# Kernel tuning notes

Hardware: AMD Instinct MI355X
Metric: run time of the kernel (lower is better)

## Reference

```python
import jax, jax.numpy as jnp
import numpy as np

N_KERNELS = 5
MUL_FACTOR = 2.0


def setup_inputs() -> dict:
    key = jax.random.key(0)
    X = jax.random.normal(key, (4096, 64), dtype=jnp.float32)
    # bandwidth multipliers: mul_factor ** (arange(K) - K//2)
    bandwidth_multipliers = (MUL_FACTOR ** (jnp.arange(N_KERNELS) - N_KERNELS // 2)).astype(jnp.float32)
    return {"X": X, "bandwidth_multipliers": bandwidth_multipliers}


def reference(X, bandwidth_multipliers):
    # squared pairwise euclidean distances: ||x_i||^2 + ||x_j||^2 - 2 x_i . x_j
    sq_norms = jnp.sum(X * X, axis=-1)                      # [N]
    gram = X @ X.T                                          # [N, N]
    L2 = jnp.maximum(sq_norms[:, None] + sq_norms[None, :] - 2.0 * gram, 0.0)  # [N, N]

    # bandwidth estimate uses .data in torch -> stop_gradient
    n = X.shape[0]
    bw = jax.lax.stop_gradient(L2.sum()) / (n * n - n)

    # sum over K bandwidth-scaled RBF kernels
    scales = bw * bandwidth_multipliers                     # [K]
    out = jnp.sum(jnp.exp(-L2[None, :, :] / scales[:, None, None]), axis=0)  # [N, N]
    return out
```

## Files before the change

kernel.cpp:

```cpp
#include <hip/hip_runtime.h>
#include <hip/hip_bf16.h>
#include <math.h>

#define N 4096
#define PB 32

typedef __attribute__((ext_vector_type(8))) short short8;
typedef __attribute__((ext_vector_type(4))) float floatx4;

__device__ float g_ws[PB * 66];
__device__ float g_nrm[N];
__device__ uint4 g_X[N * 8];

__device__ inline unsigned bfpk(float a, float b) {
    unsigned ua = __float_as_uint(a), ub = __float_as_uint(b);
    ua = (ua + 0x7fffu + ((ua >> 16) & 1u)) >> 16;
    ub = (ub + 0x7fffu + ((ub >> 16) & 1u)) >> 16;
    return ua | (ub << 16);
}

__device__ inline uint4 pack8(float4 f0, float4 f1) {
    uint4 r;
    r.x = bfpk(f0.x, f0.y);
    r.y = bfpk(f0.z, f0.w);
    r.z = bfpk(f1.x, f1.y);
    r.w = bfpk(f1.z, f1.w);
    return r;
}

__global__ __launch_bounds__(256) void prep_kernel(const float* __restrict__ X) {
    __shared__ float sm[256];
    __shared__ float ssum[4];
    const int lane = threadIdx.x & 63, w = threadIdx.x >> 6;
    const int b = blockIdx.x;

    const int row0 = b * 128 + w * 32;
    float mloc = 0.f, Sloc = 0.f;
    #pragma unroll
    for (int rr = 0; rr < 32; ++rr) {
        float x = X[(size_t)(row0 + rr) * 64 + lane];
        mloc += x; Sloc += x * x;
    }
    sm[threadIdx.x] = mloc;
    #pragma unroll
    for (int off = 1; off < 64; off <<= 1) Sloc += __shfl_xor(Sloc, off, 64);
    if (lane == 0) ssum[w] = Sloc;
    __syncthreads();
    if (threadIdx.x < 64) {
        g_ws[b * 66 + threadIdx.x] =
            sm[threadIdx.x] + sm[64 + threadIdx.x] + sm[128 + threadIdx.x] + sm[192 + threadIdx.x];
    } else if (threadIdx.x == 64) {
        g_ws[b * 66 + 64] = ssum[0] + ssum[1] + ssum[2] + ssum[3];
    }

    const int r = b * 128 + (threadIdx.x >> 1);
    const int h = threadIdx.x & 1;
    const float4* pr = (const float4*)(X + (size_t)r * 64 + h * 32);
    float4 f0 = pr[0], f1 = pr[1], f2 = pr[2], f3 = pr[3];
    float4 f4 = pr[4], f5 = pr[5], f6 = pr[6], f7 = pr[7];
    float nh = f0.x*f0.x + f0.y*f0.y + f0.z*f0.z + f0.w*f0.w
             + f1.x*f1.x + f1.y*f1.y + f1.z*f1.z + f1.w*f1.w
             + f2.x*f2.x + f2.y*f2.y + f2.z*f2.z + f2.w*f2.w
             + f3.x*f3.x + f3.y*f3.y + f3.z*f3.z + f3.w*f3.w
             + f4.x*f4.x + f4.y*f4.y + f4.z*f4.z + f4.w*f4.w
             + f5.x*f5.x + f5.y*f5.y + f5.z*f5.z + f5.w*f5.w
             + f6.x*f6.x + f6.y*f6.y + f6.z*f6.z + f6.w*f6.w
             + f7.x*f7.x + f7.y*f7.y + f7.z*f7.z + f7.w*f7.w;
    nh += __shfl_xor(nh, 1, 64);
    if (h == 0) g_nrm[r] = nh;
    const int sw = r & 7;
    g_X[r * 8 + ((4*h + 0) ^ sw)] = pack8(f0, f1);
    g_X[r * 8 + ((4*h + 1) ^ sw)] = pack8(f2, f3);
    g_X[r * 8 + ((4*h + 2) ^ sw)] = pack8(f4, f5);
    g_X[r * 8 + ((4*h + 3) ^ sw)] = pack8(f6, f7);
}

__global__ __launch_bounds__(256) void rbf_kernel(float* __restrict__ out) {
    __shared__ uint4 lB[1024];

    const int t_ = threadIdx.x;
    const int b  = blockIdx.x;

    int I, J, h;
    if (b < 64) {
        I = J = b >> 1; h = b & 1;
    } else {
        int t = (b - 64) >> 1; h = (b - 64) & 1;
        int i = (int)((63.0f - sqrtf((float)(3969 - 8 * t))) * 0.5f);
        while (31 * (i + 1) - ((i + 1) * i) / 2 <= t) ++i;
        while (31 * i - (i * (i - 1)) / 2 > t) --i;
        int oi = 31 * i - (i * (i - 1)) / 2;
        I = i; J = i + 1 + (t - oi);
    }
    const int rowBase = I * 128 + h * 64;
    const int colBase = J * 128;
    const bool offdiag = (I != J);

    #pragma unroll
    for (int i = 0; i < 4; ++i)
        lB[i * 256 + t_] = g_X[J * 1024 + i * 256 + t_];

    const int lane = t_ & 63;
    const int wave = t_ >> 6;
    const int lr = lane & 15, q = lane >> 4;

    const int r1g = rowBase + wave * 16 + lr;
    short8 a0 = *reinterpret_cast<const short8*>(&g_X[r1g * 8 + ((q    ) ^ (r1g & 7))]);
    short8 a1 = *reinterpret_cast<const short8*>(&g_X[r1g * 8 + ((q + 4) ^ (r1g & 7))]);

    const int rb = wave * 16 + q * 4;
    float sr0 = g_nrm[rowBase + rb], sr1 = g_nrm[rowBase + rb + 1];
    float sr2 = g_nrm[rowBase + rb + 2], sr3 = g_nrm[rowBase + rb + 3];
    float sc0 = g_nrm[colBase + lr],       sc1 = g_nrm[colBase + 16 + lr];
    float sc2 = g_nrm[colBase + 32 + lr],  sc3 = g_nrm[colBase + 48 + lr];
    float sc4 = g_nrm[colBase + 64 + lr],  sc5 = g_nrm[colBase + 80 + lr];
    float sc6 = g_nrm[colBase + 96 + lr],  sc7 = g_nrm[colBase + 112 + lr];

    float mv = 0.f;
    #pragma unroll 8
    for (int pb = 0; pb < PB; ++pb) mv += g_ws[pb * 66 + lane];
    float Sv = (lane < PB) ? g_ws[lane * 66 + 64] : 0.f;
    float mm = mv * mv;
    #pragma unroll
    for (int off = 1; off < 64; off <<= 1) {
        mm += __shfl_xor(mm, off, 64);
        Sv += __shfl_xor(Sv, off, 64);
    }
    float sumL2 = 2.0f * (float)N * Sv - 2.0f * mm;
    const float c1q = -1.4426950408889634f * 0.25f * (float)((size_t)N * N - N) / sumL2;

    __syncthreads();

    floatx4 acc[8];
    #pragma unroll
    for (int tj = 0; tj < 8; ++tj) acc[tj] = (floatx4){0.f, 0.f, 0.f, 0.f};

    #pragma unroll
    for (int tj = 0; tj < 8; ++tj) {
        int r2 = tj * 16 + lr;
        short8 b0 = *reinterpret_cast<const short8*>(&lB[8 * r2 + ((q    ) ^ (r2 & 7))]);
        short8 b1 = *reinterpret_cast<const short8*>(&lB[8 * r2 + ((q + 4) ^ (r2 & 7))]);
        acc[tj] = __builtin_amdgcn_mfma_f32_16x16x32_bf16(a0, b0, acc[tj], 0, 0, 0);
        acc[tj] = __builtin_amdgcn_mfma_f32_16x16x32_bf16(a1, b1, acc[tj], 0, 0, 0);
    }

    float* po0 = out + (size_t)(rowBase + rb + 0) * N + colBase + lr;
    float* po1 = po0 + N;
    float* po2 = po1 + N;
    float* po3 = po2 + N;
    float* pt  = out + (size_t)(colBase + lr) * N + rowBase + rb;

    #pragma unroll
    for (int tj = 0; tj < 8; ++tj) {
        float scj = (tj == 0) ? sc0 : (tj == 1) ? sc1 : (tj == 2) ? sc2 : (tj == 3) ? sc3
                  : (tj == 4) ? sc4 : (tj == 5) ? sc5 : (tj == 6) ? sc6 : sc7;
        float b0 = sr0 + scj, b1 = sr1 + scj, b2 = sr2 + scj, b3 = sr3 + scj;
        float d0 = fmaxf(fmaf(-2.0f, acc[tj][0], b0), 0.0f) * c1q;
        float d1 = fmaxf(fmaf(-2.0f, acc[tj][1], b1), 0.0f) * c1q;
        float d2 = fmaxf(fmaf(-2.0f, acc[tj][2], b2), 0.0f) * c1q;
        float d3 = fmaxf(fmaf(-2.0f, acc[tj][3], b3), 0.0f) * c1q;
        float u0 = __builtin_amdgcn_exp2f(d0);
        float u1 = __builtin_amdgcn_exp2f(d1);
        float u2 = __builtin_amdgcn_exp2f(d2);
        float u3 = __builtin_amdgcn_exp2f(d3);
        float s0 = u0*u0, e0 = s0*s0, e20 = e0*e0, e40 = e20*e20;
        float s1 = u1*u1, e1 = s1*s1, e21 = e1*e1, e41 = e21*e21;
        float s2 = u2*u2, e2 = s2*s2, e22 = e2*e2, e42 = e22*e22;
        float s3 = u3*u3, e3 = s3*s3, e23 = e3*e3, e43 = e23*e23;
        float v0 = e40 + e20 + e0 + s0 + u0;
        float v1 = e41 + e21 + e1 + s1 + u1;
        float v2 = e42 + e22 + e2 + s2 + u2;
        float v3 = e43 + e23 + e3 + s3 + u3;
        __builtin_nontemporal_store(v0, po0 + tj * 16);
        __builtin_nontemporal_store(v1, po1 + tj * 16);
        __builtin_nontemporal_store(v2, po2 + tj * 16);
        __builtin_nontemporal_store(v3, po3 + tj * 16);
        if (offdiag) {
            floatx4 tv = {v0, v1, v2, v3};
            __builtin_nontemporal_store(tv, reinterpret_cast<floatx4*>(pt));
        }
        pt += (size_t)16 * N;
    }
}

extern "C" void kernel_launch(void* const* d_in, const int* in_sizes, int n_in,
                              void* d_out, int out_size, void* d_ws, size_t ws_size,
                              hipStream_t stream) {
    const float* X = (const float*)d_in[0];
    float* out = (float*)d_out;
    (void)d_ws; (void)ws_size;

    prep_kernel<<<PB, 256, 0, stream>>>(X);
    rbf_kernel<<<1056, 256, 0, stream>>>(out);
}
```

Before: 93.67 us.

## Drop symmetric-tile mirroring; compute full matrix with row-strip blocks reading B from global

Replaces the upper-triangle tiling, which computed each off-diagonal tile once and wrote it plus its transpose, with a plain row-strip decomposition over all 4096x4096 outputs. Each block now handles 16 rows and half the columns, with B operands loaded straight from global memory instead of staged in LDS, and stores are ordinary rather than nontemporal. The aim is to remove the strided transposed scattered stores and the LDS sync, at the cost of doing about twice the MFMA and exp work and issuing more global loads.

```diff
diff --git a/kernel.cpp b/kernel.cpp
--- a/kernel.cpp
+++ b/kernel.cpp
@@ -75,46 +75,24 @@
     g_X[r * 8 + ((4*h + 3) ^ sw)] = pack8(f6, f7);
 }
 
-__global__ __launch_bounds__(256) void rbf_kernel(float* __restrict__ out) {
-    __shared__ uint4 lB[1024];
-
+__global__ __launch_bounds__(256, 2) void rbf_kernel(float* __restrict__ out) {
     const int t_ = threadIdx.x;
     const int b  = blockIdx.x;
+    const int lane = t_ & 63;
+    const int w  = t_ >> 6;
+    const int lr = lane & 15, q = lane >> 4;
+    const int sw = lr & 7;
 
-    int I, J, h;
-    if (b < 64) {
-        I = J = b >> 1; h = b & 1;
-    } else {
-        int t = (b - 64) >> 1; h = (b - 64) & 1;
-        int i = (int)((63.0f - sqrtf((float)(3969 - 8 * t))) * 0.5f);
-        while (31 * (i + 1) - ((i + 1) * i) / 2 <= t) ++i;
-        while (31 * i - (i * (i - 1)) / 2 > t) --i;
-        int oi = 31 * i - (i * (i - 1)) / 2;
-        I = i; J = i + 1 + (t - oi);
-    }
-    const int rowBase = I * 128 + h * 64;
-    const int colBase = J * 128;
-    const bool offdiag = (I != J);
+    const int rowBase = (b >> 1) * 16;
+    const int colW    = (b & 1) * 2048 + w * 512;
 
-    #pragma unroll
-    for (int i = 0; i < 4; ++i)
-        lB[i * 256 + t_] = g_X[J * 1024 + i * 256 + t_];
+    const int ra = rowBase + lr;
+    short8 a0 = *reinterpret_cast<const short8*>(&g_X[(size_t)ra * 8 + (q ^ sw)]);
+    short8 a1 = *reinterpret_cast<const short8*>(&g_X[(size_t)ra * 8 + ((q + 4) ^ sw)]);
 
-    const int lane = t_ & 63;
-    const int wave = t_ >> 6;
-    const int lr = lane & 15, q = lane >> 4;
-
-    const int r1g = rowBase + wave * 16 + lr;
-    short8 a0 = *reinterpret_cast<const short8*>(&g_X[r1g * 8 + ((q    ) ^ (r1g & 7))]);
-    short8 a1 = *reinterpret_cast<const short8*>(&g_X[r1g * 8 + ((q + 4) ^ (r1g & 7))]);
-
-    const int rb = wave * 16 + q * 4;
-    float sr0 = g_nrm[rowBase + rb], sr1 = g_nrm[rowBase + rb + 1];
+    const int rb = q * 4;
+    float sr0 = g_nrm[rowBase + rb],     sr1 = g_nrm[rowBase + rb + 1];
     float sr2 = g_nrm[rowBase + rb + 2], sr3 = g_nrm[rowBase + rb + 3];
-    float sc0 = g_nrm[colBase + lr],       sc1 = g_nrm[colBase + 16 + lr];
-    float sc2 = g_nrm[colBase + 32 + lr],  sc3 = g_nrm[colBase + 48 + lr];
-    float sc4 = g_nrm[colBase + 64 + lr],  sc5 = g_nrm[colBase + 80 + lr];
-    float sc6 = g_nrm[colBase + 96 + lr],  sc7 = g_nrm[colBase + 112 + lr];
 
     float mv = 0.f;
     #pragma unroll 8
@@ -129,57 +107,48 @@
     float sumL2 = 2.0f * (float)N * Sv - 2.0f * mm;
     const float c1q = -1.4426950408889634f * 0.25f * (float)((size_t)N * N - N) / sumL2;
 
-    __syncthreads();
+    #pragma unroll 1
+    for (int c = 0; c < 4; ++c) {
+        const int cb = colW + c * 128;
 
-    floatx4 acc[8];
-    #pragma unroll
-    for (int tj = 0; tj < 8; ++tj) acc[tj] = (floatx4){0.f, 0.f, 0.f, 0.f};
+        floatx4 acc[8];
+        #pragma unroll
+        for (int tj = 0; tj < 8; ++tj) acc[tj] = (floatx4){0.f, 0.f, 0.f, 0.f};
 
-    #pragma unroll
-    for (int tj = 0; tj < 8; ++tj) {
-        int r2 = tj * 16 + lr;
-        short8 b0 = *reinterpret_cast<const short8*>(&lB[8 * r2 + ((q    ) ^ (r2 & 7))]);
-        short8 b1 = *reinterpret_cast<const short8*>(&lB[8 * r2 + ((q + 4) ^ (r2 & 7))]);
-        acc[tj] = __builtin_amdgcn_mfma_f32_16x16x32_bf16(a0, b0, acc[tj], 0, 0, 0);
-        acc[tj] = __builtin_amdgcn_mfma_f32_16x16x32_bf16(a1, b1, acc[tj], 0, 0, 0);
-    }
+        #pragma unroll
+        for (int tj = 0; tj < 8; ++tj) {
+            int rc = cb + tj * 16 + lr;
+            short8 b0 = *reinterpret_cast<const short8*>(&g_X[(size_t)rc * 8 + (q ^ sw)]);
+            short8 b1 = *reinterpret_cast<const short8*>(&g_X[(size_t)rc * 8 + ((q + 4) ^ sw)]);
+            acc[tj] = __builtin_amdgcn_mfma_f32_16x16x32_bf16(a0, b0, acc[tj], 0, 0, 0);
+            acc[tj] = __builtin_amdgcn_mfma_f32_16x16x32_bf16(a1, b1, acc[tj], 0, 0, 0);
+        }
 
-    float* po0 = out + (size_t)(rowBase + rb + 0) * N + colBase + lr;
-    float* po1 = po0 + N;
-    float* po2 = po1 + N;
-    float* po3 = po2 + N;
-    float* pt  = out + (size_t)(colBase + lr) * N + rowBase + rb;
+        float* po0 = out + (size_t)(rowBase + rb) * N + cb + lr;
+        float* po1 = po0 + N;
+        float* po2 = po1 + N;
+        float* po3 = po2 + N;
 
-    #pragma unroll
-    for (int tj = 0; tj < 8; ++tj) {
-        float scj = (tj == 0) ? sc0 : (tj == 1) ? sc1 : (tj == 2) ? sc2 : (tj == 3) ? sc3
-                  : (tj == 4) ? sc4 : (tj == 5) ? sc5 : (tj == 6) ? sc6 : sc7;
-        float b0 = sr0 + scj, b1 = sr1 + scj, b2 = sr2 + scj, b3 = sr3 + scj;
-        float d0 = fmaxf(fmaf(-2.0f, acc[tj][0], b0), 0.0f) * c1q;
-        float d1 = fmaxf(fmaf(-2.0f, acc[tj][1], b1), 0.0f) * c1q;
-        float d2 = fmaxf(fmaf(-2.0f, acc[tj][2], b2), 0.0f) * c1q;
-        float d3 = fmaxf(fmaf(-2.0f, acc[tj][3], b3), 0.0f) * c1q;
-        float u0 = __builtin_amdgcn_exp2f(d0);
-        float u1 = __builtin_amdgcn_exp2f(d1);
-        float u2 = __builtin_amdgcn_exp2f(d2);
-        float u3 = __builtin_amdgcn_exp2f(d3);
-        float s0 = u0*u0, e0 = s0*s0, e20 = e0*e0, e40 = e20*e20;
-        float s1 = u1*u1, e1 = s1*s1, e21 = e1*e1, e41 = e21*e21;
-        float s2 = u2*u2, e2 = s2*s2, e22 = e2*e2, e42 = e22*e22;
-        float s3 = u3*u3, e3 = s3*s3, e23 = e3*e3, e43 = e23*e23;
-        float v0 = e40 + e20 + e0 + s0 + u0;
-        float v1 = e41 + e21 + e1 + s1 + u1;
-        float v2 = e42 + e22 + e2 + s2 + u2;
-        float v3 = e43 + e23 + e3 + s3 + u3;
-        __builtin_nontemporal_store(v0, po0 + tj * 16);
-        __builtin_nontemporal_store(v1, po1 + tj * 16);
-        __builtin_nontemporal_store(v2, po2 + tj * 16);
-        __builtin_nontemporal_store(v3, po3 + tj * 16);
-        if (offdiag) {
-            floatx4 tv = {v0, v1, v2, v3};
-            __builtin_nontemporal_store(tv, reinterpret_cast<floatx4*>(pt));
+        #pragma unroll
+        for (int tj = 0; tj < 8; ++tj) {
+            float scj = g_nrm[cb + tj * 16 + lr];
+            float d0 = fmaxf(sr0 + scj - 2.0f * acc[tj][0], 0.0f) * c1q;
+            float d1 = fmaxf(sr1 + scj - 2.0f * acc[tj][1], 0.0f) * c1q;
+            float d2 = fmaxf(sr2 + scj - 2.0f * acc[tj][2], 0.0f) * c1q;
+            float d3 = fmaxf(sr3 + scj - 2.0f * acc[tj][3], 0.0f) * c1q;
+            float u0 = __builtin_amdgcn_exp2f(d0);
+            float u1 = __builtin_amdgcn_exp2f(d1);
+            float u2 = __builtin_amdgcn_exp2f(d2);
+            float u3 = __builtin_amdgcn_exp2f(d3);
+            float s0 = u0*u0, e0 = s0*s0, e20 = e0*e0, e40 = e20*e20;
+            float s1 = u1*u1, e1 = s1*s1, e21 = e1*e1, e41 = e21*e21;
+            float s2 = u2*u2, e2 = s2*s2, e22 = e2*e2, e42 = e22*e22;
+            float s3 = u3*u3, e3 = s3*s3, e23 = e3*e3, e43 = e23*e23;
+            po0[tj * 16] = e40 + e20 + e0 + s0 + u0;
+            po1[tj * 16] = e41 + e21 + e1 + s1 + u1;
+            po2[tj * 16] = e42 + e22 + e2 + s2 + u2;
+            po3[tj * 16] = e43 + e23 + e3 + s3 + u3;
         }
-        pt += (size_t)16 * N;
     }
 }
 
@@ -191,5 +160,5 @@
     (void)d_ws; (void)ws_size;
 
     prep_kernel<<<PB, 256, 0, stream>>>(X);
-    rbf_kernel<<<1056, 256, 0, stream>>>(out);
+    rbf_kernel<<<512, 256, 0, stream>>>(out);
 }
```

Measured after the change: 88.70 us. -5.3%, faster.
